# Optimization experiments

Hardware: AMD Instinct MI355X
Metric: run time of the kernel (lower is better)

Reference implementation:

```python
import jax, jax.numpy as jnp
import numpy as np

MODES = 128
WIDTH = 128
L_SEG = 20
M_CHEB = 8


def _cft_mag(x):
    # x: [B, C, N] real. Faithful port of vectorized_batched_cft_decomposed
    # (L=20 segments, M=8 Chebyshev nodes), restricted to the first MODES
    # frequencies (the only ones consumed downstream). Returns mean-|CFT|
    # over channels: [B, MODES]. Output is detached in the original code.
    n = x.shape[-1]
    t = jnp.linspace(0.0, 1.0, n)
    freqs = jnp.arange(MODES, dtype=jnp.float32)  # rfftfreq(n, d=1/n)[:MODES]
    seg_len = 1.0 / L_SEG
    a = jnp.linspace(0.0, 1.0, L_SEG + 1)[:-1]  # [L] segment starts
    k = jnp.arange(M_CHEB, dtype=jnp.float32)
    nodes = -jnp.cos((2.0 * k + 1.0) * jnp.pi / (2.0 * M_CHEB))  # [M]
    T = jnp.cos(k[:, None] * jnp.arccos(nodes)[None, :])  # [M(k), M(node)]
    w_prime = freqs * (2.0 * jnp.pi * seg_len / 2.0)  # [F]
    exp_q = jnp.exp(-1j * nodes[:, None] * w_prime[None, :])  # [M, F]
    cheb_w = (T @ exp_q) * (seg_len / 2.0)  # [M, F] complex
    shift = jnp.exp(-1j * 2.0 * jnp.pi * freqs[None, :] * a[:, None])  # [L, F]
    W = shift[:, None, :] * cheb_w[None, :, :]  # [L, M, F]
    # quadrature sample points and linear interpolation from the grid t
    t_seg = a[:, None] + seg_len / 2.0 * (nodes[None, :] + 1.0)  # [L, M]
    right = jnp.minimum(jnp.searchsorted(t, t_seg.reshape(-1)), n - 1).reshape(L_SEG, M_CHEB)
    left = jnp.maximum(right - 1, 0)
    tl, tr = t[left], t[right]
    denom = jnp.where(tr - tl == 0.0, 1.0, tr - tl)
    w_r = (t_seg - tl) / denom
    w_l = 1.0 - w_r
    sig = w_l[None, None] * x[:, :, left] + w_r[None, None] * x[:, :, right]  # [B,C,L,M]
    spec = jnp.einsum('bclm,lmf->bcf', sig.astype(jnp.complex64), W)  # [B,C,F]
    spec = jax.lax.stop_gradient(spec)  # .detach() in the original
    return jnp.mean(jnp.abs(spec), axis=1)  # [B, MODES]


def _forward(x, fc0_W, fc0_b, gate_W, gate_b, wA_re, wA_im, wB_re, wB_im,
             conv_W, conv_b, fc1_W, fc1_b, fc2_W, fc2_b):
    B, N, _ = x.shape
    grid = jnp.broadcast_to(jnp.linspace(0.0, 1.0, N)[None, :, None], (B, N, 1))
    h = jnp.concatenate([x, grid], axis=-1) @ fc0_W.T + fc0_b  # [B,N,W]
    h = h.transpose(0, 2, 1)  # [B,W,N]
    n_f = N // 2 + 1
    for i in range(4):
        mag = _cft_mag(h)  # [B, MODES], detached
        gate = jax.nn.sigmoid(mag @ gate_W[i].T + gate_b[i])  # [B, W]
        # weights1 = gate*A + (1-gate)*B, then the original einsum
        # 'bix,bioy->box' sums weights over the mode axis y; fold that sum
        # into the (in,out) matrices first.
        wA = (wA_re[i] + 1j * wA_im[i]).sum(-1)  # [in, out]
        wB = (wB_re[i] + 1j * wB_im[i]).sum(-1)
        Wg = gate[:, None, :] * wA[None] + (1.0 - gate[:, None, :]) * wB[None]  # [B,in,out]
        h_ft = jnp.fft.rfft(h)  # [B,W,n_f]
        out_modes = jnp.einsum('bif,bio->bof', h_ft[:, :, :MODES], Wg)
        out_ft = jnp.zeros((B, WIDTH, n_f), jnp.complex64).at[:, :, :MODES].set(out_modes)
        x1 = jnp.fft.irfft(out_ft, n=N)  # [B,W,N]
        x2 = jnp.einsum('bcn,oc->bon', h, conv_W[i]) + conv_b[i][None, :, None]
        h = x1 + x2
        if i < 3:
            h = jax.nn.gelu(h, approximate=False)
    h = h.transpose(0, 2, 1)  # [B,N,W]
    h = jax.nn.gelu(h @ fc1_W.T + fc1_b, approximate=False)
    return h @ fc2_W.T + fc2_b  # [B,N,1]


def setup_inputs() -> dict:
    key = jax.random.key(0)
    ks = jax.random.split(key, 16)
    B, N = 64, 4096
    scale = 1.0 / (WIDTH * WIDTH)
    d = {}
    d['x'] = jax.random.normal(ks[0], (B, N, 1), jnp.float32)
    d['fc0_W'] = jax.random.normal(ks[1], (WIDTH, 2), jnp.float32) * 0.1
    d['fc0_b'] = jnp.zeros((WIDTH,), jnp.float32)
    d['gate_W'] = jax.random.normal(ks[2], (4, WIDTH, MODES), jnp.float32) * 0.05
    d['gate_b'] = jnp.zeros((4, WIDTH), jnp.float32)
    d['wA_re'] = jax.random.uniform(ks[3], (4, WIDTH, WIDTH, MODES), jnp.float32) * scale
    d['wA_im'] = jax.random.uniform(ks[4], (4, WIDTH, WIDTH, MODES), jnp.float32) * scale
    d['wB_re'] = jax.random.uniform(ks[5], (4, WIDTH, WIDTH, MODES), jnp.float32) * scale
    d['wB_im'] = jax.random.uniform(ks[6], (4, WIDTH, WIDTH, MODES), jnp.float32) * scale
    d['conv_W'] = jax.random.normal(ks[7], (4, WIDTH, WIDTH), jnp.float32) * 0.05
    d['conv_b'] = jnp.zeros((4, WIDTH), jnp.float32)
    d['fc1_W'] = jax.random.normal(ks[8], (128, WIDTH), jnp.float32) * 0.05
    d['fc1_b'] = jnp.zeros((128,), jnp.float32)
    d['fc2_W'] = jax.random.normal(ks[9], (1, 128), jnp.float32) * 0.05
    d['fc2_b'] = jnp.zeros((1,), jnp.float32)
    return d


def reference(x, fc0_W, fc0_b, gate_W, gate_b, wA_re, wA_im, wB_re, wB_im,
              conv_W, conv_b, fc1_W, fc1_b, fc2_W, fc2_b):
    return _forward(x, fc0_W, fc0_b, gate_W, gate_b, wA_re, wA_im, wB_re, wB_im,
                    conv_W, conv_b, fc1_W, fc1_b, fc2_W, fc2_b)
```

## Files before the change

kernel.cpp:

```cpp
#include <hip/hip_runtime.h>
#include <math.h>

#define B_SZ 64
#define WID 128
#define NPT 4096
#define MODES 128
#define LSEG 20
#define MCH 8
#define LM 160

typedef _Float16 half8 __attribute__((ext_vector_type(8)));
typedef float f32x4 __attribute__((ext_vector_type(4)));

#define LO_SCALE 2048.0f
#define LO_INV   (1.0f/2048.0f)

static constexpr size_t BY_F    = 0;
static constexpr size_t BY_wsum = BY_F + 8388608;
static constexpr size_t BY_Wcre = BY_wsum + 1048576;
static constexpr size_t BY_Wcim = BY_Wcre + 81920;
static constexpr size_t BY_wl   = BY_Wcim + 81920;
static constexpr size_t BY_wr   = BY_wl + 1024;
static constexpr size_t BY_li   = BY_wr + 1024;
static constexpr size_t BY_magp = BY_li + 1024;
static constexpr size_t BY_gate = BY_magp + 524288;
static constexpr size_t BY_hh   = BY_gate + 32768;
static constexpr size_t BY_hl   = BY_hh + 67108864;
static constexpr size_t BY_Tfh  = BY_hl + 67108864;
static constexpr size_t BY_Tfl  = BY_Tfh + 2097152;
static constexpr size_t BY_Tih  = BY_Tfl + 2097152;
static constexpr size_t BY_Til  = BY_Tih + 2097152;
static constexpr size_t BY_Xh   = BY_Til + 2097152;
static constexpr size_t BY_Xl   = BY_Xh + 4194304;
static constexpr size_t BY_cWh  = BY_Xl + 4194304;
static constexpr size_t BY_cWl  = BY_cWh + 131072;
static constexpr size_t BY_f1h  = BY_cWl + 131072;
static constexpr size_t BY_f1l  = BY_f1h + 32768;
static constexpr size_t BY_end  = BY_f1l + 32768;

__device__ __forceinline__ float gelu_f(float x){
    return 0.5f*x*(1.0f+erff(x*0.70710678118654752f));
}
__device__ __forceinline__ void split_f16(float v, _Float16& hi, _Float16& lo){
    hi = (_Float16)v;
    lo = (_Float16)((v - (float)hi)*LO_SCALE);
}

__global__ void k_tables(_Float16* __restrict__ Tffh, _Float16* __restrict__ Tffl,
                         _Float16* __restrict__ Tifh, _Float16* __restrict__ Tifl){
    int idx = blockIdx.x*256 + threadIdx.x;
    int n = idx >> 8, k2 = idx & 255;
    int f = k2 >> 1;
    int m = (n*f) & 4095;
    double th = (double)m * (3.14159265358979323846/2048.0);
    double s, c; sincos(th, &s, &c);
    float vf = (k2&1) ? (float)(-s) : (float)c;
    {
        _Float16 h1,l1; split_f16(vf, h1, l1);
        int ct = k2>>4, ck = n>>5;
        int lane = (((n>>3)&3)<<4) | (k2&15);
        int j = n & 7;
        size_t off = (((size_t)(ct*128 + ck))<<9) + lane*8 + j;
        Tffh[off] = h1; Tffl[off] = l1;
    }
    float vi;
    if (k2 == 0)      vi = 1.0f;
    else if (k2 == 1) vi = 0.0f;
    else              vi = vf;
    {
        _Float16 h2,l2; split_f16(vi, h2, l2);
        int nt = n>>4, ck2 = k2>>5;
        int lane = (((k2>>3)&3)<<4) | (n&15);
        int j = k2 & 7;
        size_t off = (((size_t)(nt*8 + ck2))<<9) + lane*8 + j;
        Tifh[off] = h2; Tifl[off] = l2;
    }
}

__global__ void k_cft_tables(float* __restrict__ Wre, float* __restrict__ Wim,
                             float* __restrict__ wl, float* __restrict__ wr,
                             int* __restrict__ li){
    int idx = blockIdx.x*128 + threadIdx.x;
    if (idx >= LM*MODES) return;
    int lm = idx >> 7;  int f = idx & 127;
    int l = lm / MCH, m = lm % MCH;
    const double PI = 3.14159265358979323846;
    double nodes[8], Tm[8];
    #pragma unroll
    for (int j=0;j<8;j++){
        nodes[j] = -cos((2.0*j+1.0)*PI/16.0);
        Tm[j] = cos((double)m * acos(nodes[j]));
    }
    double wp = (double)f * PI * 0.05;
    double cwre=0.0, cwim=0.0;
    #pragma unroll
    for (int j=0;j<8;j++){
        double sj, cj; sincos(nodes[j]*wp, &sj, &cj);
        cwre += Tm[j]*cj;
        cwim -= Tm[j]*sj;
    }
    cwre *= 0.025; cwim *= 0.025;
    int r = (f*l) % 20;
    double sa = 2.0*PI*(double)r/20.0;
    double shre = cos(sa), shim = -sin(sa);
    Wre[lm*128+f] = (float)(shre*cwre - shim*cwim);
    Wim[lm*128+f] = (float)(shre*cwim + shim*cwre);
    if (f == 0){
        double v = (double)l/20.0 + 0.025*(nodes[m]+1.0);
        int rr = (int)ceil(v*4095.0);
        if (rr > 4095) rr = 4095;
        if (rr < 1) rr = 1;
        int le = rr-1;
        double tl = (double)le/4095.0, tr = (double)rr/4095.0;
        double wrv = (v - tl)/(tr - tl);
        li[lm] = le;
        wl[lm] = (float)(1.0 - wrv);
        wr[lm] = (float)wrv;
    }
}

__global__ void k_wsum(const float* __restrict__ wAre, const float* __restrict__ wAim,
                       const float* __restrict__ wBre, const float* __restrict__ wBim,
                       float* __restrict__ out){
    int row  = blockIdx.x*4 + (threadIdx.x>>6);
    int lane = threadIdx.x & 63;
    const float* src = (blockIdx.y==0)?wAre:(blockIdx.y==1)?wAim:(blockIdx.y==2)?wBre:wBim;
    float v = src[(size_t)row*128 + lane] + src[(size_t)row*128 + 64 + lane];
    #pragma unroll
    for (int o=32;o>0;o>>=1) v += __shfl_down(v, o);
    if (lane==0) out[(size_t)blockIdx.y*65536 + row] = v;
}

__global__ void k_wsplit(const float* __restrict__ convW, const float* __restrict__ fc1W,
                         _Float16* __restrict__ cWh, _Float16* __restrict__ cWl,
                         _Float16* __restrict__ f1h, _Float16* __restrict__ f1l){
    int idx = blockIdx.x*256 + threadIdx.x;
    if (idx < 65536){
        _Float16 hi,lo; split_f16(convW[idx], hi, lo);
        cWh[idx]=hi; cWl[idx]=lo;
    } else {
        int j = idx - 65536;
        _Float16 hi,lo; split_f16(fc1W[j], hi, lo);
        f1h[j]=hi; f1l[j]=lo;
    }
}

__global__ void k_h0(const float* __restrict__ x, const float* __restrict__ w0,
                     const float* __restrict__ b0,
                     _Float16* __restrict__ hh, _Float16* __restrict__ hl){
    int idx = blockIdx.x*256 + threadIdx.x;
    int n8 = idx & 511;
    int w  = (idx >> 9) & 127;
    int b  = idx >> 16;
    int n0 = n8*8;
    float w00 = w0[w*2], w01 = w0[w*2+1], bb = b0[w];
    const float* xr = &x[((size_t)b<<12) + n0];
    float4 x0 = *reinterpret_cast<const float4*>(xr);
    float4 x1 = *reinterpret_cast<const float4*>(xr+4);
    float xv[8]={x0.x,x0.y,x0.z,x0.w,x1.x,x1.y,x1.z,x1.w};
    half8 vh, vl;
    #pragma unroll
    for (int q=0;q<8;q++){
        float g = (float)(n0+q) * (1.0f/4095.0f);
        float v = xv[q]*w00 + g*w01 + bb;
        _Float16 hi,lo; split_f16(v,hi,lo);
        vh[q]=hi; vl[q]=lo;
    }
    size_t o = ((size_t)(b*128+w))*4096 + n0;
    *reinterpret_cast<half8*>(&hh[o]) = vh;
    *reinterpret_cast<half8*>(&hl[o]) = vl;
}

__global__ void k_cft(const _Float16* __restrict__ hh, const _Float16* __restrict__ hl,
                      const float* __restrict__ Wre, const float* __restrict__ Wim,
                      const float* __restrict__ wl, const float* __restrict__ wr,
                      const int* __restrict__ li, float* __restrict__ magp){
    int b = blockIdx.x, cg = blockIdx.y;
    int f = threadIdx.x;
    __shared__ float sig[LM];
    __shared__ float swl[LM], swr[LM];
    __shared__ int   sli[LM];
    for (int s=f; s<LM; s+=128){ swl[s]=wl[s]; swr[s]=wr[s]; sli[s]=li[s]; }
    __syncthreads();
    float acc = 0.f;
    for (int cc=0; cc<8; cc++){
        int c = cg*8 + cc;
        const _Float16* rh = hh + ((size_t)(b*128+c))*4096;
        const _Float16* rl = hl + ((size_t)(b*128+c))*4096;
        for (int s=f; s<LM; s+=128){
            int le = sli[s];
            float v0 = (float)rh[le]   + (float)rl[le]*LO_INV;
            float v1 = (float)rh[le+1] + (float)rl[le+1]*LO_INV;
            sig[s] = swl[s]*v0 + swr[s]*v1;
        }
        __syncthreads();
        float re=0.f, im=0.f;
        #pragma unroll 8
        for (int s=0;s<LM;s++){
            float sv = sig[s];
            re = fmaf(sv, Wre[s*128+f], re);
            im = fmaf(sv, Wim[s*128+f], im);
        }
        acc += sqrtf(re*re+im*im);
        __syncthreads();
    }
    magp[(b*16+cg)*128 + f] = acc;
}

__global__ void k_gate(const float* __restrict__ magp, const float* __restrict__ gW,
                       const float* __restrict__ gB, float* __restrict__ gate, int layer){
    int b = blockIdx.x, w = threadIdx.x;
    __shared__ float ms[128];
    float s = 0.f;
    #pragma unroll
    for (int g=0; g<16; g++) s += magp[(b*16+g)*128 + w];
    ms[w] = s * (1.0f/128.0f);
    __syncthreads();
    const float* gwr = gW + ((size_t)layer*128 + w)*128;
    float a = gB[layer*128 + w];
    #pragma unroll 8
    for (int fq=0; fq<128; fq++) a = fmaf(ms[fq], gwr[fq], a);
    gate[b*128+w] = 1.0f/(1.0f+expf(-a));
}

__global__ __launch_bounds__(256) void k_fdft(
        const _Float16* __restrict__ hh, const _Float16* __restrict__ hl,
        const _Float16* __restrict__ Tffh, const _Float16* __restrict__ Tffl,
        float* __restrict__ F){
    __shared__ _Float16 Ah[2][64][40], Al[2][64][40];
    int id = blockIdx.x;
    int swz = (id & 7)*64 + (id >> 3);
    int bx = swz & 3, by = swz >> 2;
    int col0 = bx*64, row0 = by*64;
    int tid = threadIdx.x, lane = tid & 63, w = tid >> 6;
    int wr = (w>>1)*32, wc = (w&1)*32;
    int l15 = lane & 15, l4 = lane >> 4;
    f32x4 acc[2][2] = {}; f32x4 acc2[2][2] = {};
    int srow = tid >> 2, sseg = tid & 3;
    const _Float16* pa_h = hh + (size_t)(row0+srow)*4096 + sseg*8;
    const _Float16* pa_l = hl + (size_t)(row0+srow)*4096 + sseg*8;
    int ct0 = (col0 + wc) >> 4;
    const _Float16* pfh = Tffh + (size_t)lane*8;
    const _Float16* pfl = Tffl + (size_t)lane*8;
    half8 a0h,a0l,a1h,a1l;
    half8 bf0[4], bf1[4];
#define LOADA(xh,xl,ck) do{ \
    xh = *reinterpret_cast<const half8*>(pa_h + (size_t)(ck)*32); \
    xl = *reinterpret_cast<const half8*>(pa_l + (size_t)(ck)*32); }while(0)
#define WRITEA(xh,xl,buf) do{ \
    *reinterpret_cast<half8*>(&Ah[buf][srow][sseg*8]) = xh; \
    *reinterpret_cast<half8*>(&Al[buf][srow][sseg*8]) = xl; }while(0)
#define LOADB(dst,ck) do{ \
    dst[0] = *reinterpret_cast<const half8*>(pfh + (((size_t)(ct0  )*128 + (ck))<<9)); \
    dst[1] = *reinterpret_cast<const half8*>(pfh + (((size_t)(ct0+1)*128 + (ck))<<9)); \
    dst[2] = *reinterpret_cast<const half8*>(pfl + (((size_t)(ct0  )*128 + (ck))<<9)); \
    dst[3] = *reinterpret_cast<const half8*>(pfl + (((size_t)(ct0+1)*128 + (ck))<<9)); }while(0)
#define MMF(buf,BF) do{ \
    _Pragma("unroll") for (int i=0;i<2;i++){ \
        half8 fah = *reinterpret_cast<const half8*>(&Ah[buf][wr + i*16 + l15][l4*8]); \
        half8 fal = *reinterpret_cast<const half8*>(&Al[buf][wr + i*16 + l15][l4*8]); \
        _Pragma("unroll") for (int j=0;j<2;j++){ \
            acc[i][j]  = __builtin_amdgcn_mfma_f32_16x16x32_f16(fah, BF[j],   acc[i][j], 0,0,0); \
            acc2[i][j] = __builtin_amdgcn_mfma_f32_16x16x32_f16(fah, BF[2+j], acc2[i][j],0,0,0); \
            acc2[i][j] = __builtin_amdgcn_mfma_f32_16x16x32_f16(fal, BF[j],   acc2[i][j],0,0,0); } } }while(0)
    LOADA(a0h,a0l,0); WRITEA(a0h,a0l,0);
    LOADA(a0h,a0l,1);
    LOADA(a1h,a1l,2);
    LOADB(bf0,0); LOADB(bf1,1);
    __syncthreads();
    for (int tt=0; tt<64; ++tt){
        int t = tt*2;
        MMF(0,bf0);
        WRITEA(a0h,a0l,1);
        if (t+2 < 128) LOADB(bf0, t+2);
        if (t+3 < 128) LOADA(a0h,a0l, t+3);
        __syncthreads();
        MMF(1,bf1);
        if (t+2 < 128) WRITEA(a1h,a1l,0);
        if (t+3 < 128) LOADB(bf1, t+3);
        if (t+4 < 128) LOADA(a1h,a1l, t+4);
        __syncthreads();
    }
#undef LOADA
#undef WRITEA
#undef LOADB
#undef MMF
    #pragma unroll
    for (int i=0;i<2;i++)
        #pragma unroll
        for (int j=0;j<2;j++)
            #pragma unroll
            for (int r=0;r<4;r++){
                int row = row0 + wr + i*16 + l4*4 + r;
                int col = col0 + wc + j*16 + l15;
                F[(size_t)row*256 + col] = acc[i][j][r] + acc2[i][j][r]*LO_INV;
            }
}

__global__ __launch_bounds__(256) void k_modemix(const float* __restrict__ F,
        const float* __restrict__ wsum, const float* __restrict__ gate,
        _Float16* __restrict__ Xh, _Float16* __restrict__ Xl, int layer){
    int b = blockIdx.x, og = blockIdx.y;
    __shared__ float Fs[16][256];
    __shared__ float Wa_re[128][8], Wa_im[128][8], Wb_re[128][8], Wb_im[128][8];
    int tid = threadIdx.x;
    for (int e=tid; e<1024; e+=256){
        int i = e>>3, oo = e&7;
        size_t base = ((size_t)layer*128 + i)*128 + og*8 + oo;
        Wa_re[i][oo] = wsum[0*65536 + base];
        Wa_im[i][oo] = wsum[1*65536 + base];
        Wb_re[i][oo] = wsum[2*65536 + base];
        Wb_im[i][oo] = wsum[3*65536 + base];
    }
    int f = tid & 127, half = tid >> 7;
    float pre[4]={},pim[4]={},qre[4]={},qim[4]={};
    for (int i0=0;i0<128;i0+=16){
        for (int e=tid; e<4096; e+=256){
            int ii = e >> 8, k2 = e & 255;
            Fs[ii][k2] = F[((size_t)(b*128 + i0+ii))*256 + k2];
        }
        __syncthreads();
        #pragma unroll
        for (int ii=0; ii<16; ii++){
            float fre = Fs[ii][2*f], fim = Fs[ii][2*f+1];
            int i = i0+ii;
            #pragma unroll
            for (int q=0;q<4;q++){
                int oo = half*4+q;
                float are=Wa_re[i][oo], aim=Wa_im[i][oo];
                float bre=Wb_re[i][oo], bim=Wb_im[i][oo];
                pre[q] = fmaf(fre, are, fmaf(-fim, aim, pre[q]));
                pim[q] = fmaf(fre, aim, fmaf( fim, are, pim[q]));
                qre[q] = fmaf(fre, bre, fmaf(-fim, bim, qre[q]));
                qim[q] = fmaf(fre, bim, fmaf( fim, bre, qim[q]));
            }
        }
        __syncthreads();
    }
    #pragma unroll
    for (int q=0;q<4;q++){
        int o = og*8 + half*4 + q;
        float g = gate[b*128+o];
        float xre = g*pre[q] + (1.f-g)*qre[q];
        float xim = g*pim[q] + (1.f-g)*qim[q];
        float s = (f==0) ? (1.0f/4096.0f) : (2.0f/4096.0f);
        xre *= s; xim *= s;
        if (f==0) xim = 0.f;
        size_t base = ((size_t)(b*128+o))*256 + 2*f;
        _Float16 h1,l1; split_f16(xre,h1,l1); Xh[base]=h1;   Xl[base]=l1;
        _Float16 h2,l2; split_f16(xim,h2,l2); Xh[base+1]=h2; Xl[base+1]=l2;
    }
}

__global__ __launch_bounds__(256) void k_flayer(
    const _Float16* __restrict__ Xh, const _Float16* __restrict__ Xl,
    const _Float16* __restrict__ Tifh, const _Float16* __restrict__ Tifl,
    const _Float16* __restrict__ cWh, const _Float16* __restrict__ cWl,
    const float* __restrict__ convB,
    _Float16* __restrict__ hh, _Float16* __restrict__ hl,
    int layer, int applyGelu){
    __shared__ _Float16 As_h[2][128][40], As_l[2][128][40];
    __shared__ _Float16 Bs_h[2][64][40],  Bs_l[2][64][40];
    int n0 = blockIdx.x*64;
    int b  = blockIdx.y;
    int tid = threadIdx.x, lane = tid & 63, w = tid >> 6;
    int l15 = lane & 15, l4 = lane >> 4;
    int o0 = w*32;
    int aro = tid >> 2, asl = tid & 3;
    int ctc = tid >> 3, ctn = tid & 7;
    int ocp = ((tid >> 6) ^ (tid & 3));
    const _Float16* cA_h = cWh + (size_t)layer*16384 + (size_t)aro*128 + asl*8;
    const _Float16* cA_l = cWl + (size_t)layer*16384 + (size_t)aro*128 + asl*8;
    const _Float16* xA_h = Xh + ((size_t)(b*128 + aro))*256 + asl*8;
    const _Float16* xA_l = Xl + ((size_t)(b*128 + aro))*256 + asl*8;
    const _Float16* hB_h = hh + ((size_t)(b*128 + ctc))*4096 + n0 + ctn*8;
    const _Float16* hB_l = hl + ((size_t)(b*128 + ctc))*4096 + n0 + ctn*8;
    int nt0 = n0 >> 4;
    const _Float16* pTh = Tifh + (size_t)lane*8;
    const _Float16* pTl = Tifl + (size_t)lane*8;
    f32x4 acc[2][4] = {}; f32x4 acc2[2][4] = {};
    half8 rA[6], rB[6];
    half8 bf0[8], bf1[8];
#define LOADR(r,ck) do{ \
    if ((ck) < 4){ size_t kk = (size_t)(ck)*32; \
        r[0] = *reinterpret_cast<const half8*>(cA_h + kk); \
        r[1] = *reinterpret_cast<const half8*>(cA_l + kk); \
        r[2] = *reinterpret_cast<const half8*>(cA_h + 64*128 + kk); \
        r[3] = *reinterpret_cast<const half8*>(cA_l + 64*128 + kk); \
        r[4] = *reinterpret_cast<const half8*>(hB_h + (size_t)(ck)*32*4096); \
        r[5] = *reinterpret_cast<const half8*>(hB_l + (size_t)(ck)*32*4096); \
    } else { size_t kk = (size_t)((ck)-4)*32; \
        r[0] = *reinterpret_cast<const half8*>(xA_h + kk); \
        r[1] = *reinterpret_cast<const half8*>(xA_l + kk); \
        r[2] = *reinterpret_cast<const half8*>(xA_h + 64*256 + kk); \
        r[3] = *reinterpret_cast<const half8*>(xA_l + 64*256 + kk); } }while(0)
#define WRITER(r,buf,ck) do{ \
    *reinterpret_cast<half8*>(&As_h[buf][aro][asl*8])    = r[0]; \
    *reinterpret_cast<half8*>(&As_l[buf][aro][asl*8])    = r[1]; \
    *reinterpret_cast<half8*>(&As_h[buf][aro+64][asl*8]) = r[2]; \
    *reinterpret_cast<half8*>(&As_l[buf][aro+64][asl*8]) = r[3]; \
    if ((ck) < 4){ \
        _Pragma("unroll") for (int j2=0;j2<8;j2++){ \
            int n1 = ctn*8 + j2; \
            Bs_h[buf][n1][ocp*8 + (ctc&7)] = r[4][j2]; \
            Bs_l[buf][n1][ocp*8 + (ctc&7)] = r[5][j2]; } } }while(0)
#define LOADBF(dst,ckp) do{ \
    _Pragma("unroll") for (int j=0;j<4;j++){ \
        dst[j]   = *reinterpret_cast<const half8*>(pTh + (((size_t)((nt0+j)*8 + (ckp)))<<9)); \
        dst[4+j] = *reinterpret_cast<const half8*>(pTl + (((size_t)((nt0+j)*8 + (ckp)))<<9)); } }while(0)
#define MML(buf,ck,BF) do{ \
    half8 bh[4], bl[4]; \
    if ((ck) < 4){ \
        _Pragma("unroll") for (int j=0;j<4;j++){ \
            int n = j*16 + l15; int sl = (l4 ^ ((n>>3)&3)); \
            bh[j] = *reinterpret_cast<const half8*>(&Bs_h[buf][n][sl*8]); \
            bl[j] = *reinterpret_cast<const half8*>(&Bs_l[buf][n][sl*8]); } \
    } else { \
        _Pragma("unroll") for (int j=0;j<4;j++){ bh[j] = BF[j]; bl[j] = BF[4+j]; } } \
    _Pragma("unroll") for (int i=0;i<2;i++){ \
        half8 ah = *reinterpret_cast<const half8*>(&As_h[buf][o0+i*16+l15][l4*8]); \
        half8 al = *reinterpret_cast<const half8*>(&As_l[buf][o0+i*16+l15][l4*8]); \
        _Pragma("unroll") for (int j=0;j<4;j++){ \
            acc[i][j]  = __builtin_amdgcn_mfma_f32_16x16x32_f16(ah, bh[j], acc[i][j], 0,0,0); \
            acc2[i][j] = __builtin_amdgcn_mfma_f32_16x16x32_f16(ah, bl[j], acc2[i][j],0,0,0); \
            acc2[i][j] = __builtin_amdgcn_mfma_f32_16x16x32_f16(al, bh[j], acc2[i][j],0,0,0); } } }while(0)
    LOADR(rA, 0);
    WRITER(rA, 0, 0);
    LOADR(rA, 1);
    LOADR(rB, 2);
    __syncthreads();
    #pragma unroll
    for (int tt=0; tt<6; ++tt){
        const int t = 2*tt;
        MML(0, t, bf0);
        WRITER(rA, 1, t+1);
        if (t+2 >= 4 && t+2 < 12) LOADBF(bf0, t+2-4);
        if (t+3 < 12) LOADR(rA, t+3);
        __syncthreads();
        MML(1, t+1, bf1);
        if (t+2 < 12) WRITER(rB, 0, t+2);
        if (t+3 >= 4 && t+3 < 12) LOADBF(bf1, t+3-4);
        if (t+4 < 12) LOADR(rB, t+4);
        __syncthreads();
    }
#undef LOADR
#undef WRITER
#undef LOADBF
#undef MML
    #pragma unroll
    for (int i=0;i<2;i++)
        #pragma unroll
        for (int j=0;j<4;j++)
            #pragma unroll
            for (int r=0;r<4;r++){
                int o = o0 + i*16 + l4*4 + r;
                int n = n0 + j*16 + l15;
                float v = acc[i][j][r] + acc2[i][j][r]*LO_INV + convB[layer*128+o];
                if (applyGelu) v = gelu_f(v);
                _Float16 hi,lo; split_f16(v,hi,lo);
                size_t oi = ((size_t)(b*128+o))*4096 + n;
                hh[oi] = hi; hl[oi] = lo;
            }
}

__global__ __launch_bounds__(256) void k_head(
        const _Float16* __restrict__ hh, const _Float16* __restrict__ hl,
        const _Float16* __restrict__ f1h, const _Float16* __restrict__ f1l,
        const float* __restrict__ fc1b,
        const float* __restrict__ fc2W, const float* __restrict__ fc2b,
        float* __restrict__ out){
    __shared__ _Float16 Bch[64][136], Bcl[64][136];
    __shared__ _Float16 Ash[128][40], Asl[128][40];
    __shared__ float red[16][64];
    int n0 = blockIdx.x*64;
    int b  = blockIdx.y;
    int tid = threadIdx.x, lane = tid & 63, w = tid >> 6;
    int l15 = lane & 15, l4 = lane >> 4;
    int j0 = w*32;
    {
        int c = tid & 127, nh = tid >> 7;
        const _Float16* rh = hh + ((size_t)(b*128+c))*4096 + n0 + nh*32;
        const _Float16* rl = hl + ((size_t)(b*128+c))*4096 + n0 + nh*32;
        #pragma unroll
        for (int j=0;j<4;j++){
            half8 vhv = *reinterpret_cast<const half8*>(rh + j*8);
            half8 vlv = *reinterpret_cast<const half8*>(rl + j*8);
            #pragma unroll
            for (int q=0;q<8;q++){
                int n = nh*32 + j*8 + q;
                Bch[n][c] = vhv[q];
                Bcl[n][c] = vlv[q];
            }
        }
    }
    __syncthreads();
    int so2 = tid >> 2, sseg = tid & 3;
    f32x4 acc[2][4] = {}; f32x4 acc2[2][4] = {};
    for (int k0=0;k0<128;k0+=32){
        #pragma unroll
        for (int p=0;p<2;p++){
            int o = p*64 + so2;
            *reinterpret_cast<half8*>(&Ash[o][sseg*8]) =
                *reinterpret_cast<const half8*>(&f1h[(size_t)o*128 + k0 + sseg*8]);
            *reinterpret_cast<half8*>(&Asl[o][sseg*8]) =
                *reinterpret_cast<const half8*>(&f1l[(size_t)o*128 + k0 + sseg*8]);
        }
        __syncthreads();
        half8 ah[2],al[2],bh[4],bl[4];
        #pragma unroll
        for (int i=0;i<2;i++){
            ah[i] = *reinterpret_cast<const half8*>(&Ash[j0+i*16+l15][l4*8]);
            al[i] = *reinterpret_cast<const half8*>(&Asl[j0+i*16+l15][l4*8]);
        }
        #pragma unroll
        for (int j=0;j<4;j++){
            bh[j] = *reinterpret_cast<const half8*>(&Bch[j*16+l15][k0+l4*8]);
            bl[j] = *reinterpret_cast<const half8*>(&Bcl[j*16+l15][k0+l4*8]);
        }
        #pragma unroll
        for (int i=0;i<2;i++)
            #pragma unroll
            for (int j=0;j<4;j++){
                acc[i][j]  = __builtin_amdgcn_mfma_f32_16x16x32_f16(ah[i], bh[j], acc[i][j], 0,0,0);
                acc2[i][j] = __builtin_amdgcn_mfma_f32_16x16x32_f16(ah[i], bl[j], acc2[i][j],0,0,0);
                acc2[i][j] = __builtin_amdgcn_mfma_f32_16x16x32_f16(al[i], bh[j], acc2[i][j],0,0,0);
            }
        __syncthreads();
    }
    float part[4];
    #pragma unroll
    for (int j=0;j<4;j++) part[j] = 0.f;
    #pragma unroll
    for (int i=0;i<2;i++){
        #pragma unroll
        for (int r=0;r<4;r++){
            int jj = j0 + i*16 + l4*4 + r;
            float b1 = fc1b[jj];
            float w2 = fc2W[jj];
            #pragma unroll
            for (int j=0;j<4;j++){
                float v = acc[i][j][r] + acc2[i][j][r]*LO_INV + b1;
                part[j] = fmaf(w2, gelu_f(v), part[j]);
            }
        }
    }
    #pragma unroll
    for (int j=0;j<4;j++) red[w*4+l4][j*16+l15] = part[j];
    __syncthreads();
    if (tid < 64){
        float s = fc2b[0];
        #pragma unroll
        for (int r=0;r<16;r++) s += red[r][tid];
        out[((size_t)b<<12) + n0 + tid] = s;
    }
}

extern "C" void kernel_launch(void* const* d_in, const int* in_sizes, int n_in,
                              void* d_out, int out_size, void* d_ws, size_t ws_size,
                              hipStream_t stream) {
    const float* x     = (const float*)d_in[0];
    const float* fc0W  = (const float*)d_in[1];
    const float* fc0b  = (const float*)d_in[2];
    const float* gateW = (const float*)d_in[3];
    const float* gateB = (const float*)d_in[4];
    const float* wAre  = (const float*)d_in[5];
    const float* wAim  = (const float*)d_in[6];
    const float* wBre  = (const float*)d_in[7];
    const float* wBim  = (const float*)d_in[8];
    const float* convW = (const float*)d_in[9];
    const float* convB = (const float*)d_in[10];
    const float* fc1W  = (const float*)d_in[11];
    const float* fc1b  = (const float*)d_in[12];
    const float* fc2W  = (const float*)d_in[13];
    const float* fc2b  = (const float*)d_in[14];
    float* out = (float*)d_out;
    char*  wsb = (char*)d_ws;

    float* F    = (float*)(wsb + BY_F);
    float* wsum = (float*)(wsb + BY_wsum);
    float* Wcre = (float*)(wsb + BY_Wcre);
    float* Wcim = (float*)(wsb + BY_Wcim);
    float* wl   = (float*)(wsb + BY_wl);
    float* wr   = (float*)(wsb + BY_wr);
    int*   li   = (int*)(wsb + BY_li);
    float* magp = (float*)(wsb + BY_magp);
    float* gate = (float*)(wsb + BY_gate);
    _Float16* hh   = (_Float16*)(wsb + BY_hh);
    _Float16* hl   = (_Float16*)(wsb + BY_hl);
    _Float16* Tffh = (_Float16*)(wsb + BY_Tfh);
    _Float16* Tffl = (_Float16*)(wsb + BY_Tfl);
    _Float16* Tifh = (_Float16*)(wsb + BY_Tih);
    _Float16* Tifl = (_Float16*)(wsb + BY_Til);
    _Float16* Xh   = (_Float16*)(wsb + BY_Xh);
    _Float16* Xl   = (_Float16*)(wsb + BY_Xl);
    _Float16* cWh  = (_Float16*)(wsb + BY_cWh);
    _Float16* cWl  = (_Float16*)(wsb + BY_cWl);
    _Float16* f1h  = (_Float16*)(wsb + BY_f1h);
    _Float16* f1l  = (_Float16*)(wsb + BY_f1l);

    k_tables<<<4096, 256, 0, stream>>>(Tffh, Tffl, Tifh, Tifl);
    k_cft_tables<<<160, 128, 0, stream>>>(Wcre, Wcim, wl, wr, li);
    k_wsum<<<dim3(16384,4), 256, 0, stream>>>(wAre, wAim, wBre, wBim, wsum);
    k_wsplit<<<320, 256, 0, stream>>>(convW, fc1W, cWh, cWl, f1h, f1l);
    k_h0<<<16384, 256, 0, stream>>>(x, fc0W, fc0b, hh, hl);

    for (int layer=0; layer<4; layer++){
        k_cft<<<dim3(64,16), 128, 0, stream>>>(hh, hl, Wcre, Wcim, wl, wr, li, magp);
        k_gate<<<64, 128, 0, stream>>>(magp, gateW, gateB, gate, layer);
        k_fdft<<<512, 256, 0, stream>>>(hh, hl, Tffh, Tffl, F);
        k_modemix<<<dim3(64,16), 256, 0, stream>>>(F, wsum, gate, Xh, Xl, layer);
        k_flayer<<<dim3(64,64), 256, 0, stream>>>(Xh, Xl, Tifh, Tifl, cWh, cWl, convB,
                                                  hh, hl, layer, layer<3 ? 1:0);
    }
    k_head<<<dim3(64,64), 256, 0, stream>>>(hh, hl, f1h, f1l, fc1b, fc2W, fc2b, out);
    (void)in_sizes; (void)n_in; (void)out_size; (void)ws_size;
}
```

Measured before the change: 1.356 ms.

## Pre-swizzle conv weights and spectral input into MFMA fragment layout, drop A staging

The conv weights and mode-mixed spectrum are now written in a layout that matches the MFMA A-operand fragments, so k_flayer loads them straight from global memory into registers. This removes the A-operand shared-memory staging. The loop is split into a conv phase, which still stages h through LDS, and an inverse-DFT phase that is register double-buffered with no barriers. The aim is to cut LDS traffic and syncs, at the cost of more registers and scattered 2-byte stores in k_modemix and k_wsplit.

```diff
diff --git a/kernel.cpp b/kernel.cpp
--- a/kernel.cpp
+++ b/kernel.cpp
@@ -137,7 +137,12 @@
     int idx = blockIdx.x*256 + threadIdx.x;
     if (idx < 65536){
         _Float16 hi,lo; split_f16(convW[idx], hi, lo);
-        cWh[idx]=hi; cWl[idx]=lo;
+        int layer = idx >> 14, o = (idx >> 7) & 127, k = idx & 127;
+        int ot = o>>4, ck = k>>5;
+        int lane = ((k>>3)&3)*16 + (o&15);
+        int j = k & 7;
+        size_t off = (((size_t)((layer*8 + ot)*4 + ck))<<9) + (size_t)lane*8 + j;
+        cWh[off]=hi; cWl[off]=lo;
     } else {
         int j = idx - 65536;
         _Float16 hi,lo; split_f16(fc1W[j], hi, lo);
@@ -299,7 +304,7 @@
 
 __global__ __launch_bounds__(256) void k_modemix(const float* __restrict__ F,
         const float* __restrict__ wsum, const float* __restrict__ gate,
-        _Float16* __restrict__ Xh, _Float16* __restrict__ Xl, int layer){
+        _Float16* __restrict__ Xfh, _Float16* __restrict__ Xfl, int layer){
     int b = blockIdx.x, og = blockIdx.y;
     __shared__ float Fs[16][256];
     __shared__ float Wa_re[128][8], Wa_im[128][8], Wb_re[128][8], Wb_im[128][8];
@@ -346,107 +351,107 @@
         float s = (f==0) ? (1.0f/4096.0f) : (2.0f/4096.0f);
         xre *= s; xim *= s;
         if (f==0) xim = 0.f;
-        size_t base = ((size_t)(b*128+o))*256 + 2*f;
-        _Float16 h1,l1; split_f16(xre,h1,l1); Xh[base]=h1;   Xl[base]=l1;
-        _Float16 h2,l2; split_f16(xim,h2,l2); Xh[base+1]=h2; Xl[base+1]=l2;
+        int k2a = 2*f;
+        int ot = o >> 4, ck = k2a >> 5;
+        int lane2 = ((k2a>>3)&3)*16 + (o&15);
+        int j = k2a & 7;
+        size_t off = (((size_t)((b*8 + ot)*8 + ck))<<9) + (size_t)lane2*8 + j;
+        _Float16 h1,l1; split_f16(xre,h1,l1);
+        _Float16 h2,l2; split_f16(xim,h2,l2);
+        Xfh[off] = h1; Xfh[off+1] = h2;
+        Xfl[off] = l1; Xfl[off+1] = l2;
     }
 }
 
 __global__ __launch_bounds__(256) void k_flayer(
-    const _Float16* __restrict__ Xh, const _Float16* __restrict__ Xl,
+    const _Float16* __restrict__ Xfh, const _Float16* __restrict__ Xfl,
     const _Float16* __restrict__ Tifh, const _Float16* __restrict__ Tifl,
-    const _Float16* __restrict__ cWh, const _Float16* __restrict__ cWl,
+    const _Float16* __restrict__ cWfh, const _Float16* __restrict__ cWfl,
     const float* __restrict__ convB,
     _Float16* __restrict__ hh, _Float16* __restrict__ hl,
     int layer, int applyGelu){
-    __shared__ _Float16 As_h[2][128][40], As_l[2][128][40];
-    __shared__ _Float16 Bs_h[2][64][40],  Bs_l[2][64][40];
+    __shared__ _Float16 Bs_h[2][64][40], Bs_l[2][64][40];
     int n0 = blockIdx.x*64;
     int b  = blockIdx.y;
     int tid = threadIdx.x, lane = tid & 63, w = tid >> 6;
     int l15 = lane & 15, l4 = lane >> 4;
     int o0 = w*32;
-    int aro = tid >> 2, asl = tid & 3;
     int ctc = tid >> 3, ctn = tid & 7;
     int ocp = ((tid >> 6) ^ (tid & 3));
-    const _Float16* cA_h = cWh + (size_t)layer*16384 + (size_t)aro*128 + asl*8;
-    const _Float16* cA_l = cWl + (size_t)layer*16384 + (size_t)aro*128 + asl*8;
-    const _Float16* xA_h = Xh + ((size_t)(b*128 + aro))*256 + asl*8;
-    const _Float16* xA_l = Xl + ((size_t)(b*128 + aro))*256 + asl*8;
     const _Float16* hB_h = hh + ((size_t)(b*128 + ctc))*4096 + n0 + ctn*8;
     const _Float16* hB_l = hl + ((size_t)(b*128 + ctc))*4096 + n0 + ctn*8;
+    f32x4 acc[2][4] = {}; f32x4 acc2[2][4] = {};
+    half8 cah[4][2], cal[4][2];
+    #pragma unroll
+    for (int ck=0;ck<4;ck++)
+        #pragma unroll
+        for (int i=0;i<2;i++){
+            size_t off = (((size_t)((layer*8 + w*2 + i)*4 + ck))<<9) + (size_t)lane*8;
+            cah[ck][i] = *reinterpret_cast<const half8*>(cWfh + off);
+            cal[ck][i] = *reinterpret_cast<const half8*>(cWfl + off);
+        }
+#define WRITEB(bh_,bl_,buf) do{ \
+    _Pragma("unroll") for (int j2=0;j2<8;j2++){ \
+        int n1 = ctn*8 + j2; \
+        Bs_h[buf][n1][ocp*8 + (ctc&7)] = bh_[j2]; \
+        Bs_l[buf][n1][ocp*8 + (ctc&7)] = bl_[j2]; } }while(0)
+    half8 rbh = *reinterpret_cast<const half8*>(hB_h);
+    half8 rbl = *reinterpret_cast<const half8*>(hB_l);
+    WRITEB(rbh,rbl,0);
+    rbh = *reinterpret_cast<const half8*>(hB_h + (size_t)32*4096);
+    rbl = *reinterpret_cast<const half8*>(hB_l + (size_t)32*4096);
+    __syncthreads();
+    #pragma unroll
+    for (int ck=0;ck<4;ck++){
+        half8 bh[4], bl[4];
+        #pragma unroll
+        for (int j=0;j<4;j++){
+            int n = j*16 + l15; int sl = (l4 ^ ((n>>3)&3));
+            bh[j] = *reinterpret_cast<const half8*>(&Bs_h[ck&1][n][sl*8]);
+            bl[j] = *reinterpret_cast<const half8*>(&Bs_l[ck&1][n][sl*8]);
+        }
+        #pragma unroll
+        for (int i=0;i<2;i++)
+            #pragma unroll
+            for (int j=0;j<4;j++){
+                acc[i][j]  = __builtin_amdgcn_mfma_f32_16x16x32_f16(cah[ck][i], bh[j], acc[i][j], 0,0,0);
+                acc2[i][j] = __builtin_amdgcn_mfma_f32_16x16x32_f16(cah[ck][i], bl[j], acc2[i][j],0,0,0);
+                acc2[i][j] = __builtin_amdgcn_mfma_f32_16x16x32_f16(cal[ck][i], bh[j], acc2[i][j],0,0,0);
+            }
+        if (ck<3) WRITEB(rbh,rbl,(ck+1)&1);
+        if (ck<2){
+            rbh = *reinterpret_cast<const half8*>(hB_h + (size_t)(ck+2)*32*4096);
+            rbl = *reinterpret_cast<const half8*>(hB_l + (size_t)(ck+2)*32*4096);
+        }
+        __syncthreads();
+    }
+#undef WRITEB
     int nt0 = n0 >> 4;
-    const _Float16* pTh = Tifh + (size_t)lane*8;
-    const _Float16* pTl = Tifl + (size_t)lane*8;
-    f32x4 acc[2][4] = {}; f32x4 acc2[2][4] = {};
-    half8 rA[6], rB[6];
-    half8 bf0[8], bf1[8];
-#define LOADR(r,ck) do{ \
-    if ((ck) < 4){ size_t kk = (size_t)(ck)*32; \
-        r[0] = *reinterpret_cast<const half8*>(cA_h + kk); \
-        r[1] = *reinterpret_cast<const half8*>(cA_l + kk); \
-        r[2] = *reinterpret_cast<const half8*>(cA_h + 64*128 + kk); \
-        r[3] = *reinterpret_cast<const half8*>(cA_l + 64*128 + kk); \
-        r[4] = *reinterpret_cast<const half8*>(hB_h + (size_t)(ck)*32*4096); \
-        r[5] = *reinterpret_cast<const half8*>(hB_l + (size_t)(ck)*32*4096); \
-    } else { size_t kk = (size_t)((ck)-4)*32; \
-        r[0] = *reinterpret_cast<const half8*>(xA_h + kk); \
-        r[1] = *reinterpret_cast<const half8*>(xA_l + kk); \
-        r[2] = *reinterpret_cast<const half8*>(xA_h + 64*256 + kk); \
-        r[3] = *reinterpret_cast<const half8*>(xA_l + 64*256 + kk); } }while(0)
-#define WRITER(r,buf,ck) do{ \
-    *reinterpret_cast<half8*>(&As_h[buf][aro][asl*8])    = r[0]; \
-    *reinterpret_cast<half8*>(&As_l[buf][aro][asl*8])    = r[1]; \
-    *reinterpret_cast<half8*>(&As_h[buf][aro+64][asl*8]) = r[2]; \
-    *reinterpret_cast<half8*>(&As_l[buf][aro+64][asl*8]) = r[3]; \
-    if ((ck) < 4){ \
-        _Pragma("unroll") for (int j2=0;j2<8;j2++){ \
-            int n1 = ctn*8 + j2; \
-            Bs_h[buf][n1][ocp*8 + (ctc&7)] = r[4][j2]; \
-            Bs_l[buf][n1][ocp*8 + (ctc&7)] = r[5][j2]; } } }while(0)
-#define LOADBF(dst,ckp) do{ \
+    half8 xah[2][2], xal[2][2], xbh[2][4], xbl[2][4];
+#define LOADI(s,ck) do{ \
+    _Pragma("unroll") for (int i=0;i<2;i++){ \
+        size_t off = (((size_t)((b*8 + w*2 + i)*8 + (ck)))<<9) + (size_t)lane*8; \
+        xah[s][i] = *reinterpret_cast<const half8*>(Xfh + off); \
+        xal[s][i] = *reinterpret_cast<const half8*>(Xfl + off); } \
     _Pragma("unroll") for (int j=0;j<4;j++){ \
-        dst[j]   = *reinterpret_cast<const half8*>(pTh + (((size_t)((nt0+j)*8 + (ckp)))<<9)); \
-        dst[4+j] = *reinterpret_cast<const half8*>(pTl + (((size_t)((nt0+j)*8 + (ckp)))<<9)); } }while(0)
-#define MML(buf,ck,BF) do{ \
-    half8 bh[4], bl[4]; \
-    if ((ck) < 4){ \
-        _Pragma("unroll") for (int j=0;j<4;j++){ \
-            int n = j*16 + l15; int sl = (l4 ^ ((n>>3)&3)); \
-            bh[j] = *reinterpret_cast<const half8*>(&Bs_h[buf][n][sl*8]); \
-            bl[j] = *reinterpret_cast<const half8*>(&Bs_l[buf][n][sl*8]); } \
-    } else { \
-        _Pragma("unroll") for (int j=0;j<4;j++){ bh[j] = BF[j]; bl[j] = BF[4+j]; } } \
-    _Pragma("unroll") for (int i=0;i<2;i++){ \
-        half8 ah = *reinterpret_cast<const half8*>(&As_h[buf][o0+i*16+l15][l4*8]); \
-        half8 al = *reinterpret_cast<const half8*>(&As_l[buf][o0+i*16+l15][l4*8]); \
-        _Pragma("unroll") for (int j=0;j<4;j++){ \
-            acc[i][j]  = __builtin_amdgcn_mfma_f32_16x16x32_f16(ah, bh[j], acc[i][j], 0,0,0); \
-            acc2[i][j] = __builtin_amdgcn_mfma_f32_16x16x32_f16(ah, bl[j], acc2[i][j],0,0,0); \
-            acc2[i][j] = __builtin_amdgcn_mfma_f32_16x16x32_f16(al, bh[j], acc2[i][j],0,0,0); } } }while(0)
-    LOADR(rA, 0);
-    WRITER(rA, 0, 0);
-    LOADR(rA, 1);
-    LOADR(rB, 2);
-    __syncthreads();
-    #pragma unroll
-    for (int tt=0; tt<6; ++tt){
-        const int t = 2*tt;
-        MML(0, t, bf0);
-        WRITER(rA, 1, t+1);
-        if (t+2 >= 4 && t+2 < 12) LOADBF(bf0, t+2-4);
-        if (t+3 < 12) LOADR(rA, t+3);
-        __syncthreads();
-        MML(1, t+1, bf1);
-        if (t+2 < 12) WRITER(rB, 0, t+2);
-        if (t+3 >= 4 && t+3 < 12) LOADBF(bf1, t+3-4);
-        if (t+4 < 12) LOADR(rB, t+4);
-        __syncthreads();
-    }
-#undef LOADR
-#undef WRITER
-#undef LOADBF
-#undef MML
+        size_t off = (((size_t)((nt0 + j)*8 + (ck)))<<9) + (size_t)lane*8; \
+        xbh[s][j] = *reinterpret_cast<const half8*>(Tifh + off); \
+        xbl[s][j] = *reinterpret_cast<const half8*>(Tifl + off); } }while(0)
+    LOADI(0,0); LOADI(1,1);
+    #pragma unroll
+    for (int ck=0;ck<8;ck++){
+        const int s = ck&1;
+        #pragma unroll
+        for (int i=0;i<2;i++)
+            #pragma unroll
+            for (int j=0;j<4;j++){
+                acc[i][j]  = __builtin_amdgcn_mfma_f32_16x16x32_f16(xah[s][i], xbh[s][j], acc[i][j], 0,0,0);
+                acc2[i][j] = __builtin_amdgcn_mfma_f32_16x16x32_f16(xah[s][i], xbl[s][j], acc2[i][j],0,0,0);
+                acc2[i][j] = __builtin_amdgcn_mfma_f32_16x16x32_f16(xal[s][i], xbh[s][j], acc2[i][j],0,0,0);
+            }
+        if (ck+2 < 8) LOADI(s, ck+2);
+    }
+#undef LOADI
     #pragma unroll
     for (int i=0;i<2;i++)
         #pragma unroll
@@ -591,25 +596,25 @@
     _Float16* Tffl = (_Float16*)(wsb + BY_Tfl);
     _Float16* Tifh = (_Float16*)(wsb + BY_Tih);
     _Float16* Tifl = (_Float16*)(wsb + BY_Til);
-    _Float16* Xh   = (_Float16*)(wsb + BY_Xh);
-    _Float16* Xl   = (_Float16*)(wsb + BY_Xl);
-    _Float16* cWh  = (_Float16*)(wsb + BY_cWh);
-    _Float16* cWl  = (_Float16*)(wsb + BY_cWl);
+    _Float16* Xfh  = (_Float16*)(wsb + BY_Xh);
+    _Float16* Xfl  = (_Float16*)(wsb + BY_Xl);
+    _Float16* cWfh = (_Float16*)(wsb + BY_cWh);
+    _Float16* cWfl = (_Float16*)(wsb + BY_cWl);
     _Float16* f1h  = (_Float16*)(wsb + BY_f1h);
     _Float16* f1l  = (_Float16*)(wsb + BY_f1l);
 
     k_tables<<<4096, 256, 0, stream>>>(Tffh, Tffl, Tifh, Tifl);
     k_cft_tables<<<160, 128, 0, stream>>>(Wcre, Wcim, wl, wr, li);
     k_wsum<<<dim3(16384,4), 256, 0, stream>>>(wAre, wAim, wBre, wBim, wsum);
-    k_wsplit<<<320, 256, 0, stream>>>(convW, fc1W, cWh, cWl, f1h, f1l);
+    k_wsplit<<<320, 256, 0, stream>>>(convW, fc1W, cWfh, cWfl, f1h, f1l);
     k_h0<<<16384, 256, 0, stream>>>(x, fc0W, fc0b, hh, hl);
 
     for (int layer=0; layer<4; layer++){
         k_cft<<<dim3(64,16), 128, 0, stream>>>(hh, hl, Wcre, Wcim, wl, wr, li, magp);
         k_gate<<<64, 128, 0, stream>>>(magp, gateW, gateB, gate, layer);
         k_fdft<<<512, 256, 0, stream>>>(hh, hl, Tffh, Tffl, F);
-        k_modemix<<<dim3(64,16), 256, 0, stream>>>(F, wsum, gate, Xh, Xl, layer);
-        k_flayer<<<dim3(64,64), 256, 0, stream>>>(Xh, Xl, Tifh, Tifl, cWh, cWl, convB,
+        k_modemix<<<dim3(64,16), 256, 0, stream>>>(F, wsum, gate, Xfh, Xfl, layer);
+        k_flayer<<<dim3(64,64), 256, 0, stream>>>(Xfh, Xfl, Tifh, Tifl, cWfh, cWfl, convB,
                                                   hh, hl, layer, layer<3 ? 1:0);
     }
     k_head<<<dim3(64,64), 256, 0, stream>>>(hh, hl, f1h, f1l, fc1b, fc2W, fc2b, out);
```

Result: slower. 1.451 ms (+7.0%).
